# Kernel tuning notes

Hardware: AMD Instinct MI355X
Metric: run time of the kernel (lower is better)

Reference implementation:

```python
import jax, jax.numpy as jnp
import numpy as np

B, H, W, D, DFF = 32, 40, 40, 128, 2048
S = H * W  # 1600
BN_EPS = 1e-5


def setup_inputs() -> dict:
    key = jax.random.key(0)
    ks = jax.random.split(key, 8)
    se = jax.random.normal(ks[2], (H, W, H, W), dtype=jnp.float32)
    se = se + jnp.transpose(se, (2, 3, 0, 1))  # symmetric init as in torch code
    wscale = 0.02
    return {
        "tgt": jax.random.normal(ks[0], (B, H, W, D), dtype=jnp.float32),
        "memory": jax.random.normal(ks[1], (B, H, W, D), dtype=jnp.float32),
        "score_embed": se,
        "w1": jax.random.normal(ks[3], (D, D), dtype=jnp.float32) * wscale,
        "b1": jnp.zeros((D,), jnp.float32),
        "g1": jnp.ones((2 * S,), jnp.float32),
        "be1": jnp.zeros((2 * S,), jnp.float32),
        "w2": jax.random.normal(ks[4], (DFF, 2 * S), dtype=jnp.float32) * wscale,
        "b2": jnp.zeros((DFF,), jnp.float32),
        "g2": jnp.ones((DFF,), jnp.float32),
        "be2": jnp.zeros((DFF,), jnp.float32),
        "w3": jax.random.normal(ks[5], (1, DFF), dtype=jnp.float32) * wscale,
        "b3": jnp.zeros((1,), jnp.float32),
        "g3": jnp.ones((1,), jnp.float32),
        "be3": jnp.zeros((1,), jnp.float32),
    }


def _bn_eval(x, gamma, beta):
    # BatchNorm eval mode with running_mean=0, running_var=1 (as initialized)
    return x * (gamma / jnp.sqrt(1.0 + BN_EPS)) + beta


def _l2norm(x):
    # F.normalize(p=2, dim=-1) with eps=1e-12
    return x / jnp.maximum(jnp.linalg.norm(x, axis=-1, keepdims=True), 1e-12)


def reference(tgt, memory, score_embed, w1, b1, g1, be1, w2, b2, g2, be2, w3, b3, g3, be3):
    b, h, w, d = tgt.shape
    s = h * w
    q = _l2norm(tgt.reshape(b, s, d) @ w1.T + b1)   # [B,S,D]
    k = _l2norm(memory.reshape(b, s, d) @ w1.T + b1)
    gate = jax.nn.sigmoid(score_embed.reshape(s, s))  # [S,S]
    attn = jnp.einsum("bsd,btd->bst", q, k) * gate    # [B,S,S]
    m1 = attn.max(axis=1)  # max over dim 1 -> [B,S]
    m2 = attn.max(axis=2)  # max over dim 2 -> [B,S]
    x = jnp.concatenate([m1, m2], axis=1)  # [B,2S]
    x = _bn_eval(x, g1, be1)
    x = x @ w2.T + b2        # [B,DFF]
    x = jax.nn.relu(_bn_eval(x, g2, be2))
    x = x @ w3.T + b3        # [B,1]
    x = _bn_eval(x, g3, be3)
    return x.squeeze(-1)     # [B]
```

## Files before the change

kernel.cpp:

```cpp
#include <hip/hip_runtime.h>
#include <hip/hip_bf16.h>

#define BB 32
#define SS 1600
#define DD 128
#define DFFN 2048
#define S2N 3200
#define RS 136

typedef __attribute__((ext_vector_type(8))) short short8;
typedef __attribute__((ext_vector_type(4))) float floatx4;
typedef unsigned int u32;
typedef unsigned short u16;

__device__ __forceinline__ u32 encf(float f) {
  u32 u = __float_as_uint(f);
  return (u & 0x80000000u) ? ~u : (u | 0x80000000u);
}
__device__ __forceinline__ float decf(u32 e) {
  u32 u = (e & 0x80000000u) ? (e & 0x7fffffffu) : ~e;
  return __uint_as_float(u);
}
__device__ __forceinline__ u16 f2b(float x) {
  __hip_bfloat16 h = __float2bfloat16(x);
  return __builtin_bit_cast(u16, h);
}
__device__ __forceinline__ float b2f(u16 h) { return __uint_as_float(((u32)h) << 16); }
__device__ __forceinline__ float sigm(float x) { return 1.f / (1.f + __expf(-x)); }

__global__ __launch_bounds__(256) void k_init(const float* __restrict__ se,
                                              u16* __restrict__ gT2,
                                              const float* __restrict__ w1,
                                              u16* __restrict__ w1b,
                                              u32* __restrict__ m1u,
                                              u32* __restrict__ m2u) {
  int tid = threadIdx.x;
  int bid = blockIdx.x;
  int i = bid * 256 + tid;
  if (i < BB * SS) {
    m1u[i] = 0u;
    m2u[i] = 0u;
  }
  if (i < 4096) {
    float4 v = ((const float4*)w1)[i];
    ushort4 o;
    o.x = f2b(v.x); o.y = f2b(v.y); o.z = f2b(v.z); o.w = f2b(v.w);
    ((ushort4*)w1b)[i] = o;
  }
  if (bid < 676) {
    int r2 = bid >> 2, mi = bid & 3;
    int sy = r2 / 13, tx = r2 - sy * 13;
    int s0 = min(sy * 128, SS - 128);
    int t0 = min(tx * 128, SS - 128);
    int lane = tid & 63, wv = tid >> 6;
    int wr = wv >> 1, wc = wv & 1;
    int l15 = lane & 15, lg = lane >> 4;
    int srow = s0 + wr * 64 + mi * 16 + lg * 4;
    u16* tb = gT2 + (size_t)r2 * 16384 + wv * 4096 + mi * 4 * 256 + lane * 4;
    for (int ni = 0; ni < 4; ++ni) {
      int tcol = t0 + wc * 64 + ni * 16 + l15;
      const float* sp = se + (size_t)srow * SS + tcol;
      ushort4 o;
      o.x = f2b(sigm(sp[0]));
      o.y = f2b(sigm(sp[SS]));
      o.z = f2b(sigm(sp[2 * SS]));
      o.w = f2b(sigm(sp[3 * SS]));
      *(ushort4*)(tb + ni * 256) = o;
    }
  }
}

__global__ __launch_bounds__(256) void k_proj(const float* __restrict__ tgt,
                                              const float* __restrict__ memin,
                                              const u16* __restrict__ w1b,
                                              const float* __restrict__ b1,
                                              u16* __restrict__ qb, u16* __restrict__ kb) {
  __shared__ u16 sA[128 * RS];
  __shared__ float sq[128];
  int tid = threadIdx.x;
  long row0 = (long)blockIdx.x * 128;
  const float* src;
  u16* dst;
  if (row0 < (long)BB * SS) { src = tgt + row0 * DD; dst = qb + row0 * DD; }
  else { src = memin + (row0 - (long)BB * SS) * DD; dst = kb + (row0 - (long)BB * SS) * DD; }

  for (int p = 0; p < 16; ++p) {
    int r = p * 8 + (tid >> 5);
    int c4 = (tid & 31) * 4;
    float4 v = *(const float4*)(src + r * DD + c4);
    u32 p0 = (u32)f2b(v.x) | ((u32)f2b(v.y) << 16);
    u32 p1 = (u32)f2b(v.z) | ((u32)f2b(v.w) << 16);
    *(u32*)&sA[r * RS + c4] = p0;
    *(u32*)&sA[r * RS + c4 + 2] = p1;
  }
  if (tid < 128) sq[tid] = 0.f;
  __syncthreads();

  int lane = tid & 63, wv = tid >> 6;
  int wr = wv >> 1, wc = wv & 1;
  int l15 = lane & 15, lg = lane >> 4;

  floatx4 acc[4][4];
  for (int mi = 0; mi < 4; ++mi)
    for (int ni = 0; ni < 4; ++ni) acc[mi][ni] = (floatx4){0.f, 0.f, 0.f, 0.f};

  for (int kc = 0; kc < 4; ++kc) {
    int k0 = kc * 32 + lg * 8;
    short8 af[4], bfr[4];
    for (int mi = 0; mi < 4; ++mi) af[mi] = *(const short8*)&sA[(wr * 64 + mi * 16 + l15) * RS + k0];
    for (int ni = 0; ni < 4; ++ni)
      bfr[ni] = *(const short8*)(w1b + (size_t)(wc * 64 + ni * 16 + l15) * DD + k0);
    for (int mi = 0; mi < 4; ++mi)
      for (int ni = 0; ni < 4; ++ni)
        acc[mi][ni] = __builtin_amdgcn_mfma_f32_16x16x32_bf16(af[mi], bfr[ni], acc[mi][ni], 0, 0, 0);
  }

  float bvals[4];
  for (int ni = 0; ni < 4; ++ni) bvals[ni] = b1[wc * 64 + ni * 16 + l15];
  for (int mi = 0; mi < 4; ++mi)
    for (int r = 0; r < 4; ++r) {
      float s = 0.f;
      for (int ni = 0; ni < 4; ++ni) {
        float v = acc[mi][ni][r] + bvals[ni];
        acc[mi][ni][r] = v;
        s += v * v;
      }
      s += __shfl_xor(s, 1); s += __shfl_xor(s, 2);
      s += __shfl_xor(s, 4); s += __shfl_xor(s, 8);
      if (l15 == 0) atomicAdd(&sq[wr * 64 + mi * 16 + lg * 4 + r], s);
    }
  __syncthreads();

  for (int mi = 0; mi < 4; ++mi)
    for (int r = 0; r < 4; ++r) {
      int row = wr * 64 + mi * 16 + lg * 4 + r;
      float scale = 1.f / fmaxf(sqrtf(sq[row]), 1e-12f);
      for (int ni = 0; ni < 4; ++ni)
        sA[row * RS + wc * 64 + ni * 16 + l15] = f2b(acc[mi][ni][r] * scale);
    }
  __syncthreads();
  for (int p = 0; p < 16; ++p) {
    int r = p * 8 + (tid >> 5);
    int c4 = (tid & 31) * 4;
    uint2 val = *(const uint2*)&sA[r * RS + c4];
    *(uint2*)(dst + r * DD + c4) = val;
  }
}

__global__ __launch_bounds__(256, 3) void k_attn(const u16* __restrict__ qb,
                                                 const u16* __restrict__ kb,
                                                 const u16* __restrict__ gT2,
                                                 u32* __restrict__ m1u, u32* __restrict__ m2u) {
  __shared__ u16 sK[128 * RS];
  __shared__ float scmax[2][128];
  __shared__ float srmax[2][128];
  int tid = threadIdx.x;
  int n = blockIdx.x;
  int id = (n & 7) * 676 + (n >> 3);
  int b = id / 169;
  int r2 = id - b * 169;
  int sy = r2 / 13, tx = r2 - sy * 13;
  int s0 = min(sy * 128, SS - 128);
  int t0 = min(tx * 128, SS - 128);
  int lane = tid & 63, wv = tid >> 6;
  int wr = wv >> 1, wc = wv & 1;
  int l15 = lane & 15, lg = lane >> 4;
  const size_t base = (size_t)b * SS * DD;

  short8 qf[4][4];
  {
    const u16* qp = qb + base + (size_t)(s0 + wr * 64 + l15) * DD + lg * 8;
    for (int mi = 0; mi < 4; ++mi)
      for (int kc = 0; kc < 4; ++kc)
        qf[mi][kc] = *(const short8*)(qp + mi * 16 * DD + kc * 32);
  }
  {
    int rr0 = tid >> 4;
    int c8 = (tid & 15) * 8;
    const u16* kp = kb + base + (size_t)(t0 + rr0) * DD + c8;
    u16* sp = &sK[rr0 * RS + c8];
    for (int p = 0; p < 8; ++p)
      *(uint4*)(sp + p * 16 * RS) = *(const uint4*)(kp + (size_t)p * 16 * DD);
  }
  __syncthreads();

  floatx4 acc[4][4];
  for (int mi = 0; mi < 4; ++mi)
    for (int ni = 0; ni < 4; ++ni) acc[mi][ni] = (floatx4){0.f, 0.f, 0.f, 0.f};

  for (int kc = 0; kc < 2; ++kc) {
    int k0 = kc * 32 + lg * 8;
    short8 bfr[4];
    for (int ni = 0; ni < 4; ++ni) bfr[ni] = *(const short8*)&sK[(wc * 64 + ni * 16 + l15) * RS + k0];
    for (int mi = 0; mi < 4; ++mi)
      for (int ni = 0; ni < 4; ++ni)
        acc[mi][ni] = __builtin_amdgcn_mfma_f32_16x16x32_bf16(qf[mi][kc], bfr[ni], acc[mi][ni], 0, 0, 0);
  }

  ushort4 gv[4][4];
  {
    const u16* gbase = gT2 + (size_t)r2 * 16384 + wv * 4096 + lane * 4;
    for (int mi = 0; mi < 4; ++mi)
      for (int ni = 0; ni < 4; ++ni)
        gv[mi][ni] = *(const ushort4*)(gbase + (mi * 4 + ni) * 256);
  }

  for (int kc = 2; kc < 4; ++kc) {
    int k0 = kc * 32 + lg * 8;
    short8 bfr[4];
    for (int ni = 0; ni < 4; ++ni) bfr[ni] = *(const short8*)&sK[(wc * 64 + ni * 16 + l15) * RS + k0];
    for (int mi = 0; mi < 4; ++mi)
      for (int ni = 0; ni < 4; ++ni)
        acc[mi][ni] = __builtin_amdgcn_mfma_f32_16x16x32_bf16(qf[mi][kc], bfr[ni], acc[mi][ni], 0, 0, 0);
  }

  float rmax[4][4];
  for (int mi = 0; mi < 4; ++mi)
    for (int r = 0; r < 4; ++r) rmax[mi][r] = -1e30f;
  float cmax[4];
  for (int ni = 0; ni < 4; ++ni) cmax[ni] = -1e30f;

  for (int mi = 0; mi < 4; ++mi)
    for (int ni = 0; ni < 4; ++ni) {
      ushort4 ge = gv[mi][ni];
      float v0 = acc[mi][ni][0] * b2f(ge.x);
      float v1 = acc[mi][ni][1] * b2f(ge.y);
      float v2 = acc[mi][ni][2] * b2f(ge.z);
      float v3 = acc[mi][ni][3] * b2f(ge.w);
      rmax[mi][0] = fmaxf(rmax[mi][0], v0);
      rmax[mi][1] = fmaxf(rmax[mi][1], v1);
      rmax[mi][2] = fmaxf(rmax[mi][2], v2);
      rmax[mi][3] = fmaxf(rmax[mi][3], v3);
      cmax[ni] = fmaxf(cmax[ni], fmaxf(fmaxf(v0, v1), fmaxf(v2, v3)));
    }

  for (int ni = 0; ni < 4; ++ni) {
    cmax[ni] = fmaxf(cmax[ni], __shfl_xor(cmax[ni], 16));
    cmax[ni] = fmaxf(cmax[ni], __shfl_xor(cmax[ni], 32));
  }
  if (lane < 16)
    for (int ni = 0; ni < 4; ++ni) scmax[wr][wc * 64 + ni * 16 + l15] = cmax[ni];

  for (int mi = 0; mi < 4; ++mi)
    for (int r = 0; r < 4; ++r) {
      float v = rmax[mi][r];
      v = fmaxf(v, __shfl_xor(v, 1));
      v = fmaxf(v, __shfl_xor(v, 2));
      v = fmaxf(v, __shfl_xor(v, 4));
      v = fmaxf(v, __shfl_xor(v, 8));
      if (l15 == 0) srmax[wc][wr * 64 + mi * 16 + lg * 4 + r] = v;
    }
  __syncthreads();

  if (tid < 128) {
    float v = fmaxf(scmax[0][tid], scmax[1][tid]);
    atomicMax(&m1u[b * SS + t0 + tid], encf(v));
  } else {
    int i = tid - 128;
    float v = fmaxf(srmax[0][i], srmax[1][i]);
    atomicMax(&m2u[b * SS + s0 + i], encf(v));
  }
}

__global__ __launch_bounds__(256) void k_gemm2(const u32* __restrict__ m1u,
                                               const u32* __restrict__ m2u,
                                               const float* __restrict__ g1,
                                               const float* __restrict__ be1,
                                               const float* __restrict__ w2,
                                               float* __restrict__ hacc) {
  int tid = threadIdx.x;
  int lane = tid & 63, wv = tid >> 6;
  int f0 = blockIdx.x * 32 + wv * 8;
  int cs = blockIdx.y;
  int cr0 = cs * 800;
  const u32* msrc = (cs < 2) ? m1u : m2u;
  int mcol0 = cr0 - ((cs < 2) ? 0 : SS);
  int c_sub = lane & 15, bq = lane >> 4;
  const float bnc = rsqrtf(1.f + 1e-5f);
  float acc[8][8];
  for (int a = 0; a < 8; ++a)
    for (int c = 0; c < 8; ++c) acc[a][c] = 0.f;
  const float4 z4 = {0.f, 0.f, 0.f, 0.f};
  for (int it = 0; it < 13; ++it) {
    int coff = it * 64 + c_sub * 4;
    bool ok = coff < 800;
    int cg = cr0 + coff;
    float4 w4[8], x4[8];
    float4 gv = ok ? *(const float4*)(g1 + cg) : z4;
    float4 bv = ok ? *(const float4*)(be1 + cg) : z4;
    gv.x *= bnc; gv.y *= bnc; gv.z *= bnc; gv.w *= bnc;
    for (int jf = 0; jf < 8; ++jf)
      w4[jf] = ok ? *(const float4*)(w2 + (size_t)(f0 + jf) * S2N + cg) : z4;
    for (int j = 0; j < 8; ++j) {
      if (ok) {
        uint4 e = *(const uint4*)(msrc + (size_t)(bq * 8 + j) * SS + mcol0 + coff);
        x4[j].x = decf(e.x) * gv.x + bv.x;
        x4[j].y = decf(e.y) * gv.y + bv.y;
        x4[j].z = decf(e.z) * gv.z + bv.z;
        x4[j].w = decf(e.w) * gv.w + bv.w;
      } else {
        x4[j] = z4;
      }
    }
    for (int jf = 0; jf < 8; ++jf)
      for (int j = 0; j < 8; ++j) {
        float a = acc[jf][j];
        a = fmaf(w4[jf].x, x4[j].x, a);
        a = fmaf(w4[jf].y, x4[j].y, a);
        a = fmaf(w4[jf].z, x4[j].z, a);
        a = fmaf(w4[jf].w, x4[j].w, a);
        acc[jf][j] = a;
      }
  }
  for (int jf = 0; jf < 8; ++jf)
    for (int j = 0; j < 8; ++j) {
      float v = acc[jf][j];
      v += __shfl_xor(v, 1); v += __shfl_xor(v, 2);
      v += __shfl_xor(v, 4); v += __shfl_xor(v, 8);
      acc[jf][j] = v;
    }
  if ((lane & 15) == 0) {
    for (int jf = 0; jf < 8; ++jf)
      for (int j = 0; j < 8; ++j) {
        int b = bq * 8 + j;
        hacc[((size_t)cs * BB + b) * DFFN + f0 + jf] = acc[jf][j];
      }
  }
}

__global__ __launch_bounds__(256) void k_final(const float* __restrict__ hacc,
                                               const float* __restrict__ b2,
                                               const float* __restrict__ g2,
                                               const float* __restrict__ be2,
                                               const float* __restrict__ w3,
                                               const float* __restrict__ b3,
                                               const float* __restrict__ g3,
                                               const float* __restrict__ be3,
                                               float* __restrict__ out) {
  __shared__ float wsum[4];
  int b = blockIdx.x;
  int tid = threadIdx.x;
  float bnc = rsqrtf(1.f + 1e-5f);
  float part = 0.f;
  for (int f = tid; f < DFFN; f += 256) {
    float s = hacc[((size_t)0 * BB + b) * DFFN + f] + hacc[((size_t)1 * BB + b) * DFFN + f] +
              hacc[((size_t)2 * BB + b) * DFFN + f] + hacc[((size_t)3 * BB + b) * DFFN + f];
    s += b2[f];
    s = s * (g2[f] * bnc) + be2[f];
    s = fmaxf(s, 0.f);
    part += s * w3[f];
  }
  for (int m = 1; m < 64; m <<= 1) part += __shfl_xor(part, m);
  if ((tid & 63) == 0) wsum[tid >> 6] = part;
  __syncthreads();
  if (tid == 0) {
    float tot = wsum[0] + wsum[1] + wsum[2] + wsum[3] + b3[0];
    out[b] = tot * (g3[0] * bnc) + be3[0];
  }
}

extern "C" void kernel_launch(void* const* d_in, const int* in_sizes, int n_in,
                              void* d_out, int out_size, void* d_ws, size_t ws_size,
                              hipStream_t stream) {
  const float* tgt = (const float*)d_in[0];
  const float* memin = (const float*)d_in[1];
  const float* se = (const float*)d_in[2];
  const float* w1 = (const float*)d_in[3];
  const float* b1 = (const float*)d_in[4];
  const float* g1 = (const float*)d_in[5];
  const float* be1 = (const float*)d_in[6];
  const float* w2 = (const float*)d_in[7];
  const float* b2 = (const float*)d_in[8];
  const float* g2 = (const float*)d_in[9];
  const float* be2 = (const float*)d_in[10];
  const float* w3 = (const float*)d_in[11];
  const float* b3 = (const float*)d_in[12];
  const float* g3 = (const float*)d_in[13];
  const float* be3 = (const float*)d_in[14];
  float* out = (float*)d_out;

  char* ws = (char*)d_ws;
  const size_t OFF_GT = 0;
  const size_t OFF_W1B = 5537792;
  const size_t OFF_QB = OFF_W1B + 32768;
  const size_t OFF_KB = OFF_QB + 13107200;
  const size_t OFF_M1 = OFF_KB + 13107200;
  const size_t OFF_M2 = OFF_M1 + 204800;
  const size_t OFF_HA = OFF_M2 + 204800;
  const size_t NEEDED = OFF_HA + (size_t)4 * BB * DFFN * 4;
  if (ws_size < NEEDED) return;

  u16* gT2 = (u16*)(ws + OFF_GT);
  u16* w1b = (u16*)(ws + OFF_W1B);
  u16* qb = (u16*)(ws + OFF_QB);
  u16* kb = (u16*)(ws + OFF_KB);
  u32* m1u = (u32*)(ws + OFF_M1);
  u32* m2u = (u32*)(ws + OFF_M2);
  float* hacc = (float*)(ws + OFF_HA);

  k_init<<<676, 256, 0, stream>>>(se, gT2, w1, w1b, m1u, m2u);
  k_proj<<<800, 256, 0, stream>>>(tgt, memin, w1b, b1, qb, kb);
  k_attn<<<5408, 256, 0, stream>>>(qb, kb, gT2, m1u, m2u);
  k_gemm2<<<dim3(64, 4), 256, 0, stream>>>(m1u, m2u, g1, be1, w2, hacc);
  k_final<<<32, 256, 0, stream>>>(hacc, b2, g2, be2, w3, b3, g3, be3, out);
}
```

Measured before the change: 166.1 us.

## Reuse gate tiles across four batches and replace atomic max with partial-max reduction

Each attention block now loops over four batches and keeps the sigmoid gate fragments in registers, so each gate tile is loaded once instead of four times. The block count drops accordingly. Encoded atomicMax into global buffers is replaced by per-tile partial maxima written to scratch, followed by a new reduce kernel that also applies the first BatchNorm. This removes the buffer zeroing and the decode step in the second GEMM. Q fragments are double-buffered across the k-steps. The cost is one extra launch, extra partial-buffer traffic, and fewer blocks, which may leave an uneven tail wave.

```diff
diff --git a/kernel.cpp b/kernel.cpp
--- a/kernel.cpp
+++ b/kernel.cpp
@@ -13,14 +13,6 @@
 typedef unsigned int u32;
 typedef unsigned short u16;
 
-__device__ __forceinline__ u32 encf(float f) {
-  u32 u = __float_as_uint(f);
-  return (u & 0x80000000u) ? ~u : (u | 0x80000000u);
-}
-__device__ __forceinline__ float decf(u32 e) {
-  u32 u = (e & 0x80000000u) ? (e & 0x7fffffffu) : ~e;
-  return __uint_as_float(u);
-}
 __device__ __forceinline__ u16 f2b(float x) {
   __hip_bfloat16 h = __float2bfloat16(x);
   return __builtin_bit_cast(u16, h);
@@ -31,42 +23,34 @@
 __global__ __launch_bounds__(256) void k_init(const float* __restrict__ se,
                                               u16* __restrict__ gT2,
                                               const float* __restrict__ w1,
-                                              u16* __restrict__ w1b,
-                                              u32* __restrict__ m1u,
-                                              u32* __restrict__ m2u) {
+                                              u16* __restrict__ w1b) {
   int tid = threadIdx.x;
   int bid = blockIdx.x;
   int i = bid * 256 + tid;
-  if (i < BB * SS) {
-    m1u[i] = 0u;
-    m2u[i] = 0u;
-  }
   if (i < 4096) {
     float4 v = ((const float4*)w1)[i];
     ushort4 o;
     o.x = f2b(v.x); o.y = f2b(v.y); o.z = f2b(v.z); o.w = f2b(v.w);
     ((ushort4*)w1b)[i] = o;
   }
-  if (bid < 676) {
-    int r2 = bid >> 2, mi = bid & 3;
-    int sy = r2 / 13, tx = r2 - sy * 13;
-    int s0 = min(sy * 128, SS - 128);
-    int t0 = min(tx * 128, SS - 128);
-    int lane = tid & 63, wv = tid >> 6;
-    int wr = wv >> 1, wc = wv & 1;
-    int l15 = lane & 15, lg = lane >> 4;
-    int srow = s0 + wr * 64 + mi * 16 + lg * 4;
-    u16* tb = gT2 + (size_t)r2 * 16384 + wv * 4096 + mi * 4 * 256 + lane * 4;
-    for (int ni = 0; ni < 4; ++ni) {
-      int tcol = t0 + wc * 64 + ni * 16 + l15;
-      const float* sp = se + (size_t)srow * SS + tcol;
-      ushort4 o;
-      o.x = f2b(sigm(sp[0]));
-      o.y = f2b(sigm(sp[SS]));
-      o.z = f2b(sigm(sp[2 * SS]));
-      o.w = f2b(sigm(sp[3 * SS]));
-      *(ushort4*)(tb + ni * 256) = o;
-    }
+  int r2 = bid >> 2, mi = bid & 3;
+  int sy = r2 / 13, tx = r2 - sy * 13;
+  int s0 = min(sy * 128, SS - 128);
+  int t0 = min(tx * 128, SS - 128);
+  int lane = tid & 63, wv = tid >> 6;
+  int wr = wv >> 1, wc = wv & 1;
+  int l15 = lane & 15, lg = lane >> 4;
+  int srow = s0 + wr * 64 + mi * 16 + lg * 4;
+  u16* tb = gT2 + (size_t)r2 * 16384 + wv * 4096 + mi * 4 * 256 + lane * 4;
+  for (int ni = 0; ni < 4; ++ni) {
+    int tcol = t0 + wc * 64 + ni * 16 + l15;
+    const float* sp = se + (size_t)srow * SS + tcol;
+    ushort4 o;
+    o.x = f2b(sigm(sp[0]));
+    o.y = f2b(sigm(sp[SS]));
+    o.z = f2b(sigm(sp[2 * SS]));
+    o.w = f2b(sigm(sp[3 * SS]));
+    *(ushort4*)(tb + ni * 256) = o;
   }
 }
 
@@ -150,52 +134,21 @@
 __global__ __launch_bounds__(256, 3) void k_attn(const u16* __restrict__ qb,
                                                  const u16* __restrict__ kb,
                                                  const u16* __restrict__ gT2,
-                                                 u32* __restrict__ m1u, u32* __restrict__ m2u) {
+                                                 float* __restrict__ p1,
+                                                 float* __restrict__ p2) {
   __shared__ u16 sK[128 * RS];
   __shared__ float scmax[2][128];
   __shared__ float srmax[2][128];
   int tid = threadIdx.x;
   int n = blockIdx.x;
-  int id = (n & 7) * 676 + (n >> 3);
-  int b = id / 169;
-  int r2 = id - b * 169;
+  int bq = n & 7;
+  int r2 = n >> 3;
   int sy = r2 / 13, tx = r2 - sy * 13;
   int s0 = min(sy * 128, SS - 128);
   int t0 = min(tx * 128, SS - 128);
   int lane = tid & 63, wv = tid >> 6;
   int wr = wv >> 1, wc = wv & 1;
   int l15 = lane & 15, lg = lane >> 4;
-  const size_t base = (size_t)b * SS * DD;
-
-  short8 qf[4][4];
-  {
-    const u16* qp = qb + base + (size_t)(s0 + wr * 64 + l15) * DD + lg * 8;
-    for (int mi = 0; mi < 4; ++mi)
-      for (int kc = 0; kc < 4; ++kc)
-        qf[mi][kc] = *(const short8*)(qp + mi * 16 * DD + kc * 32);
-  }
-  {
-    int rr0 = tid >> 4;
-    int c8 = (tid & 15) * 8;
-    const u16* kp = kb + base + (size_t)(t0 + rr0) * DD + c8;
-    u16* sp = &sK[rr0 * RS + c8];
-    for (int p = 0; p < 8; ++p)
-      *(uint4*)(sp + p * 16 * RS) = *(const uint4*)(kp + (size_t)p * 16 * DD);
-  }
-  __syncthreads();
-
-  floatx4 acc[4][4];
-  for (int mi = 0; mi < 4; ++mi)
-    for (int ni = 0; ni < 4; ++ni) acc[mi][ni] = (floatx4){0.f, 0.f, 0.f, 0.f};
-
-  for (int kc = 0; kc < 2; ++kc) {
-    int k0 = kc * 32 + lg * 8;
-    short8 bfr[4];
-    for (int ni = 0; ni < 4; ++ni) bfr[ni] = *(const short8*)&sK[(wc * 64 + ni * 16 + l15) * RS + k0];
-    for (int mi = 0; mi < 4; ++mi)
-      for (int ni = 0; ni < 4; ++ni)
-        acc[mi][ni] = __builtin_amdgcn_mfma_f32_16x16x32_bf16(qf[mi][kc], bfr[ni], acc[mi][ni], 0, 0, 0);
-  }
 
   ushort4 gv[4][4];
   {
@@ -205,67 +158,126 @@
         gv[mi][ni] = *(const ushort4*)(gbase + (mi * 4 + ni) * 256);
   }
 
-  for (int kc = 2; kc < 4; ++kc) {
-    int k0 = kc * 32 + lg * 8;
-    short8 bfr[4];
-    for (int ni = 0; ni < 4; ++ni) bfr[ni] = *(const short8*)&sK[(wc * 64 + ni * 16 + l15) * RS + k0];
-    for (int mi = 0; mi < 4; ++mi)
-      for (int ni = 0; ni < 4; ++ni)
-        acc[mi][ni] = __builtin_amdgcn_mfma_f32_16x16x32_bf16(qf[mi][kc], bfr[ni], acc[mi][ni], 0, 0, 0);
-  }
-
-  float rmax[4][4];
-  for (int mi = 0; mi < 4; ++mi)
-    for (int r = 0; r < 4; ++r) rmax[mi][r] = -1e30f;
-  float cmax[4];
-  for (int ni = 0; ni < 4; ++ni) cmax[ni] = -1e30f;
-
-  for (int mi = 0; mi < 4; ++mi)
+  int rr0 = tid >> 4;
+  int c8 = (tid & 15) * 8;
+
+  for (int bi = 0; bi < 4; ++bi) {
+    int b = bq * 4 + bi;
+    const size_t base = (size_t)b * SS * DD;
+    const u16* qp = qb + base + (size_t)(s0 + wr * 64 + l15) * DD + lg * 8;
+
+    uint4 kv[8];
+    {
+      const u16* kp = kb + base + (size_t)(t0 + rr0) * DD + c8;
+      for (int p = 0; p < 8; ++p) kv[p] = *(const uint4*)(kp + (size_t)p * 16 * DD);
+    }
+    short8 qsA[4], qsB[4];
+    for (int mi = 0; mi < 4; ++mi) qsA[mi] = *(const short8*)(qp + mi * 16 * DD);
+    {
+      u16* sp = &sK[rr0 * RS + c8];
+      for (int p = 0; p < 8; ++p) *(uint4*)(sp + p * 16 * RS) = kv[p];
+    }
+    __syncthreads();
+
+    floatx4 acc[4][4];
+    for (int mi = 0; mi < 4; ++mi)
+      for (int ni = 0; ni < 4; ++ni) acc[mi][ni] = (floatx4){0.f, 0.f, 0.f, 0.f};
+
+#define QKSTEP(KC, CUR, NXT, PRE)                                                       \
+    {                                                                                   \
+      if (PRE)                                                                          \
+        for (int mi = 0; mi < 4; ++mi)                                                  \
+          NXT[mi] = *(const short8*)(qp + mi * 16 * DD + ((KC) + 1) * 32);              \
+      int k0 = (KC)*32 + lg * 8;                                                        \
+      short8 bfr[4];                                                                    \
+      for (int ni = 0; ni < 4; ++ni)                                                    \
+        bfr[ni] = *(const short8*)&sK[(wc * 64 + ni * 16 + l15) * RS + k0];             \
+      for (int mi = 0; mi < 4; ++mi)                                                    \
+        for (int ni = 0; ni < 4; ++ni)                                                  \
+          acc[mi][ni] = __builtin_amdgcn_mfma_f32_16x16x32_bf16(CUR[mi], bfr[ni],       \
+                                                                acc[mi][ni], 0, 0, 0);  \
+    }
+    QKSTEP(0, qsA, qsB, 1)
+    QKSTEP(1, qsB, qsA, 1)
+    QKSTEP(2, qsA, qsB, 1)
+    QKSTEP(3, qsB, qsA, 0)
+#undef QKSTEP
+
+    float rmax[4][4];
+    for (int mi = 0; mi < 4; ++mi)
+      for (int r = 0; r < 4; ++r) rmax[mi][r] = -1e30f;
+    float cmax[4];
+    for (int ni = 0; ni < 4; ++ni) cmax[ni] = -1e30f;
+
+    for (int mi = 0; mi < 4; ++mi)
+      for (int ni = 0; ni < 4; ++ni) {
+        ushort4 ge = gv[mi][ni];
+        float v0 = acc[mi][ni][0] * b2f(ge.x);
+        float v1 = acc[mi][ni][1] * b2f(ge.y);
+        float v2 = acc[mi][ni][2] * b2f(ge.z);
+        float v3 = acc[mi][ni][3] * b2f(ge.w);
+        rmax[mi][0] = fmaxf(rmax[mi][0], v0);
+        rmax[mi][1] = fmaxf(rmax[mi][1], v1);
+        rmax[mi][2] = fmaxf(rmax[mi][2], v2);
+        rmax[mi][3] = fmaxf(rmax[mi][3], v3);
+        cmax[ni] = fmaxf(cmax[ni], fmaxf(fmaxf(v0, v1), fmaxf(v2, v3)));
+      }
+
     for (int ni = 0; ni < 4; ++ni) {
-      ushort4 ge = gv[mi][ni];
-      float v0 = acc[mi][ni][0] * b2f(ge.x);
-      float v1 = acc[mi][ni][1] * b2f(ge.y);
-      float v2 = acc[mi][ni][2] * b2f(ge.z);
-      float v3 = acc[mi][ni][3] * b2f(ge.w);
-      rmax[mi][0] = fmaxf(rmax[mi][0], v0);
-      rmax[mi][1] = fmaxf(rmax[mi][1], v1);
-      rmax[mi][2] = fmaxf(rmax[mi][2], v2);
-      rmax[mi][3] = fmaxf(rmax[mi][3], v3);
-      cmax[ni] = fmaxf(cmax[ni], fmaxf(fmaxf(v0, v1), fmaxf(v2, v3)));
-    }
-
-  for (int ni = 0; ni < 4; ++ni) {
-    cmax[ni] = fmaxf(cmax[ni], __shfl_xor(cmax[ni], 16));
-    cmax[ni] = fmaxf(cmax[ni], __shfl_xor(cmax[ni], 32));
-  }
-  if (lane < 16)
-    for (int ni = 0; ni < 4; ++ni) scmax[wr][wc * 64 + ni * 16 + l15] = cmax[ni];
-
-  for (int mi = 0; mi < 4; ++mi)
-    for (int r = 0; r < 4; ++r) {
-      float v = rmax[mi][r];
-      v = fmaxf(v, __shfl_xor(v, 1));
-      v = fmaxf(v, __shfl_xor(v, 2));
-      v = fmaxf(v, __shfl_xor(v, 4));
-      v = fmaxf(v, __shfl_xor(v, 8));
-      if (l15 == 0) srmax[wc][wr * 64 + mi * 16 + lg * 4 + r] = v;
-    }
-  __syncthreads();
-
-  if (tid < 128) {
-    float v = fmaxf(scmax[0][tid], scmax[1][tid]);
-    atomicMax(&m1u[b * SS + t0 + tid], encf(v));
+      cmax[ni] = fmaxf(cmax[ni], __shfl_xor(cmax[ni], 16));
+      cmax[ni] = fmaxf(cmax[ni], __shfl_xor(cmax[ni], 32));
+    }
+    if (lane < 16)
+      for (int ni = 0; ni < 4; ++ni) scmax[wr][wc * 64 + ni * 16 + lane] = cmax[ni];
+
+    for (int mi = 0; mi < 4; ++mi)
+      for (int r = 0; r < 4; ++r) {
+        float v = rmax[mi][r];
+        v = fmaxf(v, __shfl_xor(v, 1));
+        v = fmaxf(v, __shfl_xor(v, 2));
+        v = fmaxf(v, __shfl_xor(v, 4));
+        v = fmaxf(v, __shfl_xor(v, 8));
+        if (l15 == 0) srmax[wc][wr * 64 + mi * 16 + lg * 4 + r] = v;
+      }
+    __syncthreads();
+
+    size_t pbase = ((size_t)(b * 13 + sy) * 13 + tx) * 128;
+    if (tid < 128) {
+      p1[pbase + tid] = fmaxf(scmax[0][tid], scmax[1][tid]);
+    } else {
+      int i2 = tid - 128;
+      p2[pbase + i2] = fmaxf(srmax[0][i2], srmax[1][i2]);
+    }
+  }
+}
+
+__global__ __launch_bounds__(256) void k_reduce(const float* __restrict__ p1,
+                                                const float* __restrict__ p2,
+                                                const float* __restrict__ g1,
+                                                const float* __restrict__ be1,
+                                                float* __restrict__ xb) {
+  int i = blockIdx.x * 256 + threadIdx.x;
+  if (i >= BB * S2N) return;
+  int bb = i / S2N, c = i - bb * S2N;
+  float v = -1e30f;
+  if (c < SS) {
+    int t = c;
+    int txc = min(t >> 7, 12);
+    int col = t - ((txc == 12) ? (SS - 128) : txc * 128);
+    const float* pp = p1 + ((size_t)(bb * 13) * 13 + txc) * 128 + col;
+    for (int sy = 0; sy < 13; ++sy) v = fmaxf(v, pp[(size_t)sy * 13 * 128]);
   } else {
-    int i = tid - 128;
-    float v = fmaxf(srmax[0][i], srmax[1][i]);
-    atomicMax(&m2u[b * SS + s0 + i], encf(v));
-  }
-}
-
-__global__ __launch_bounds__(256) void k_gemm2(const u32* __restrict__ m1u,
-                                               const u32* __restrict__ m2u,
-                                               const float* __restrict__ g1,
-                                               const float* __restrict__ be1,
+    int s = c - SS;
+    int syc = min(s >> 7, 12);
+    int col = s - ((syc == 12) ? (SS - 128) : syc * 128);
+    const float* pp = p2 + ((size_t)(bb * 13 + syc) * 13) * 128 + col;
+    for (int tx = 0; tx < 13; ++tx) v = fmaxf(v, pp[(size_t)tx * 128]);
+  }
+  float bnc = rsqrtf(1.f + 1e-5f);
+  xb[i] = v * (g1[c] * bnc) + be1[c];
+}
+
+__global__ __launch_bounds__(256) void k_gemm2(const float* __restrict__ xb,
                                                const float* __restrict__ w2,
                                                float* __restrict__ hacc) {
   int tid = threadIdx.x;
@@ -273,10 +285,7 @@
   int f0 = blockIdx.x * 32 + wv * 8;
   int cs = blockIdx.y;
   int cr0 = cs * 800;
-  const u32* msrc = (cs < 2) ? m1u : m2u;
-  int mcol0 = cr0 - ((cs < 2) ? 0 : SS);
   int c_sub = lane & 15, bq = lane >> 4;
-  const float bnc = rsqrtf(1.f + 1e-5f);
   float acc[8][8];
   for (int a = 0; a < 8; ++a)
     for (int c = 0; c < 8; ++c) acc[a][c] = 0.f;
@@ -284,24 +293,12 @@
   for (int it = 0; it < 13; ++it) {
     int coff = it * 64 + c_sub * 4;
     bool ok = coff < 800;
-    int cg = cr0 + coff;
+    int c = cr0 + coff;
     float4 w4[8], x4[8];
-    float4 gv = ok ? *(const float4*)(g1 + cg) : z4;
-    float4 bv = ok ? *(const float4*)(be1 + cg) : z4;
-    gv.x *= bnc; gv.y *= bnc; gv.z *= bnc; gv.w *= bnc;
     for (int jf = 0; jf < 8; ++jf)
-      w4[jf] = ok ? *(const float4*)(w2 + (size_t)(f0 + jf) * S2N + cg) : z4;
-    for (int j = 0; j < 8; ++j) {
-      if (ok) {
-        uint4 e = *(const uint4*)(msrc + (size_t)(bq * 8 + j) * SS + mcol0 + coff);
-        x4[j].x = decf(e.x) * gv.x + bv.x;
-        x4[j].y = decf(e.y) * gv.y + bv.y;
-        x4[j].z = decf(e.z) * gv.z + bv.z;
-        x4[j].w = decf(e.w) * gv.w + bv.w;
-      } else {
-        x4[j] = z4;
-      }
-    }
+      w4[jf] = ok ? *(const float4*)(w2 + (size_t)(f0 + jf) * S2N + c) : z4;
+    for (int j = 0; j < 8; ++j)
+      x4[j] = ok ? *(const float4*)(xb + (size_t)(bq * 8 + j) * S2N + c) : z4;
     for (int jf = 0; jf < 8; ++jf)
       for (int j = 0; j < 8; ++j) {
         float a = acc[jf][j];
@@ -384,23 +381,26 @@
   const size_t OFF_W1B = 5537792;
   const size_t OFF_QB = OFF_W1B + 32768;
   const size_t OFF_KB = OFF_QB + 13107200;
-  const size_t OFF_M1 = OFF_KB + 13107200;
-  const size_t OFF_M2 = OFF_M1 + 204800;
-  const size_t OFF_HA = OFF_M2 + 204800;
-  const size_t NEEDED = OFF_HA + (size_t)4 * BB * DFFN * 4;
+  const size_t OFF_P1 = OFF_KB + 13107200;
+  const size_t OFF_P2 = OFF_P1 + 2768896;
+  const size_t NEEDED = OFF_P2 + 2768896;
+  const size_t OFF_XB = 0;
+  const size_t OFF_HA = 409600;
   if (ws_size < NEEDED) return;
 
   u16* gT2 = (u16*)(ws + OFF_GT);
   u16* w1b = (u16*)(ws + OFF_W1B);
   u16* qb = (u16*)(ws + OFF_QB);
   u16* kb = (u16*)(ws + OFF_KB);
-  u32* m1u = (u32*)(ws + OFF_M1);
-  u32* m2u = (u32*)(ws + OFF_M2);
+  float* p1 = (float*)(ws + OFF_P1);
+  float* p2 = (float*)(ws + OFF_P2);
+  float* xb = (float*)(ws + OFF_XB);
   float* hacc = (float*)(ws + OFF_HA);
 
-  k_init<<<676, 256, 0, stream>>>(se, gT2, w1, w1b, m1u, m2u);
+  k_init<<<676, 256, 0, stream>>>(se, gT2, w1, w1b);
   k_proj<<<800, 256, 0, stream>>>(tgt, memin, w1b, b1, qb, kb);
-  k_attn<<<5408, 256, 0, stream>>>(qb, kb, gT2, m1u, m2u);
-  k_gemm2<<<dim3(64, 4), 256, 0, stream>>>(m1u, m2u, g1, be1, w2, hacc);
+  k_attn<<<1352, 256, 0, stream>>>(qb, kb, gT2, p1, p2);
+  k_reduce<<<400, 256, 0, stream>>>(p1, p2, g1, be1, xb);
+  k_gemm2<<<dim3(64, 4), 256, 0, stream>>>(xb, w2, hacc);
   k_final<<<32, 256, 0, stream>>>(hacc, b2, g2, be2, w3, b3, g3, be3, out);
 }
```

After: 216.1 us. 1.3x slower.
